# Performance work log

Measured on AMD Instinct MI355X. Metric: run time of the kernel, lower is better.

## Reference

```python
import jax, jax.numpy as jnp
import numpy as np
from math import sqrt

B, S, E, H = 2, 2048, 768, 12
DH = E // H
W = 256            # one-sided attention window (attention_window=512)
G = 16             # number of global tokens (positions 0..G-1 in every batch row)
PAD = 128          # last PAD tokens per row are padding (masked)
FF = 3072          # SwiGLU intermediate size
NEG = -1e9
EPS = 1e-5


def _ln(x, g, b):
    m = jnp.mean(x, axis=-1, keepdims=True)
    v = jnp.var(x, axis=-1, keepdims=True)
    return (x - m) * jax.lax.rsqrt(v + EPS) * g + b


def _rope(x, t):
    # x: [B,H,S,DH]; t: [B,S] float 'set positions'
    half = DH // 2
    inv_freq = 1.0 / (10000.0 ** (jnp.arange(half, dtype=jnp.float32) / half))
    ang = t[:, None, :, None] * inv_freq            # [B,1,S,half]
    cos, sin = jnp.cos(ang), jnp.sin(ang)
    x1, x2 = x[..., :half], x[..., half:]
    return jnp.concatenate([x1 * cos - x2 * sin, x2 * cos + x1 * sin], axis=-1)


def _heads(x):  # [B,S,E] -> [B,H,S,DH]
    return x.reshape(B, S, H, DH).transpose(0, 2, 1, 3)


def _chunk3(x):
    # [B,H,S,D] -> [B,H,C,3W,D]: for query chunk c, keys from chunks c-1,c,c+1 (zero padded)
    b, h, s, d = x.shape
    c = s // W
    xp = jnp.pad(x, ((0, 0), (0, 0), (W, W), (0, 0))).reshape(b, h, c + 2, W, d)
    return jnp.concatenate([xp[:, :, :-2], xp[:, :, 1:-1], xp[:, :, 2:]], axis=3)


def _forward(x, attention_mask, global_attention_mask,
             Wq, bq, Wk, bk, Wv, bv, Wqg, bqg, Wkg, bkg, Wvg, bvg,
             ln0_g, ln0_b, ln1_g, ln1_b, W1, W3, W2):
    C = S // W
    merged = attention_mask * (global_attention_mask + 1)   # 0 masked, 1 local, 2 global
    is_masked = merged == 0
    is_global = merged == 2
    remove = merged != 1   # keys removed from windowed attention (masked or global)

    q = _heads(x @ Wq + bq) / sqrt(DH)
    k = _heads(x @ Wk + bk)
    v = _heads(x @ Wv + bv)

    # RoPE over 'set positions': (~is_index_masked) * cumsum(is_index_global_attn)
    t = jnp.where(is_masked, 0, jnp.cumsum(is_global.astype(jnp.int32), axis=1)).astype(jnp.float32)
    q = _rope(q, t)
    k = _rope(k, t)

    # --- sliding-window (banded) scores: band[b,h,i,d] = q_i . k_{i+d-W} ---
    qc = q.reshape(B, H, C, W, DH)
    k3 = _chunk3(k)
    s3 = jnp.einsum('bhcpd,bhcqd->bhcpq', qc, k3)                     # [B,H,C,W,3W]
    didx = jnp.arange(W)[:, None] + jnp.arange(2 * W + 1)[None, :]    # [W,2W+1]
    band = jnp.take_along_axis(s3, didx[None, None, None], axis=-1)   # [B,H,C,W,2W+1]

    # mask removed keys / out-of-range positions inside the band
    rmp = jnp.pad(remove, ((0, 0), (W, W)), constant_values=True).reshape(B, C + 2, W)
    rm3 = jnp.concatenate([rmp[:, :-2], rmp[:, 1:-1], rmp[:, 2:]], axis=2)  # [B,C,3W]
    band_rm = jnp.take_along_axis(jnp.broadcast_to(rm3[:, :, None, :], (B, C, W, 3 * W)),
                                  didx[None, None], axis=-1)                # [B,C,W,2W+1]
    band = jnp.where(band_rm[:, None], NEG, band).reshape(B, H, S, 2 * W + 1)

    # --- global-key columns (keys taken from the RoPE'd local key vectors) ---
    sg = jnp.einsum('bhid,bhgd->bhig', q, k[:, :, :G])                # [B,H,S,G]

    scores = jnp.concatenate([sg, band], axis=-1)                     # [B,H,S,G+2W+1]
    probs = jax.nn.softmax(scores.astype(jnp.float32), axis=-1).astype(x.dtype)
    probs = jnp.where(is_masked[:, None, :, None], 0.0, probs)

    # --- probs @ value: global columns + band ---
    out = jnp.einsum('bhig,bhgd->bhid', probs[..., :G], v[:, :, :G])
    pl = probs[..., G:].reshape(B, H, C, W, 2 * W + 1)
    rows = jnp.broadcast_to(jnp.arange(W)[:, None], (W, 2 * W + 1))
    p3 = jnp.zeros((B, H, C, W, 3 * W), probs.dtype).at[:, :, :, rows, didx].set(pl)
    v3 = _chunk3(v)
    out = out + jnp.einsum('bhcpq,bhcqd->bhcpd', p3, v3).reshape(B, H, S, DH)
    attn = out.transpose(0, 2, 1, 3).reshape(B, S, E)

    # --- full attention for global tokens (separate global projections, no RoPE) ---
    gq = _heads(x @ Wqg + bqg)[:, :, :G] / sqrt(DH)                   # [B,H,G,DH]
    gk = _heads(x @ Wkg + bkg)
    gv = _heads(x @ Wvg + bvg)
    gs = jnp.einsum('bhgd,bhjd->bhgj', gq, gk)                        # [B,H,G,S]
    gs = jnp.where(is_masked[:, None, None, :], NEG, gs)
    gp = jax.nn.softmax(gs.astype(jnp.float32), axis=-1).astype(x.dtype)
    gout = jnp.einsum('bhgj,bhjd->bhgd', gp, gv).transpose(0, 2, 1, 3).reshape(B, G, E)
    attn = attn.at[:, :G].set(gout)

    # residual + post-LN, SwiGLU FFN, residual + post-LN (dropout = eval mode)
    h0 = _ln(x + attn, ln0_g, ln0_b)
    ffn = (jax.nn.silu(h0 @ W1) * (h0 @ W3)) @ W2
    return _ln(h0 + ffn, ln1_g, ln1_b)


def setup_inputs():
    key = jax.random.key(0)
    ks = jax.random.split(key, 12)
    x = jax.random.normal(ks[0], (B, S, E), jnp.float32)
    attention_mask = jnp.ones((B, S), jnp.int32).at[:, S - PAD:].set(0)
    global_attention_mask = jnp.zeros((B, S), jnp.int32).at[:, :G].set(1)
    sd = 0.02
    def w(k, shape):
        return jax.random.normal(k, shape, jnp.float32) * sd
    return dict(
        x=x, attention_mask=attention_mask, global_attention_mask=global_attention_mask,
        Wq=w(ks[1], (E, E)), bq=jnp.zeros((E,), jnp.float32),
        Wk=w(ks[2], (E, E)), bk=jnp.zeros((E,), jnp.float32),
        Wv=w(ks[3], (E, E)), bv=jnp.zeros((E,), jnp.float32),
        Wqg=w(ks[4], (E, E)), bqg=jnp.zeros((E,), jnp.float32),
        Wkg=w(ks[5], (E, E)), bkg=jnp.zeros((E,), jnp.float32),
        Wvg=w(ks[6], (E, E)), bvg=jnp.zeros((E,), jnp.float32),
        ln0_g=jnp.ones((E,), jnp.float32), ln0_b=jnp.zeros((E,), jnp.float32),
        ln1_g=jnp.ones((E,), jnp.float32), ln1_b=jnp.zeros((E,), jnp.float32),
        W1=w(ks[7], (E, FF)), W3=w(ks[8], (E, FF)), W2=w(ks[9], (FF, E)))


def reference(x, attention_mask, global_attention_mask, Wq, bq, Wk, bk, Wv, bv,
              Wqg, bqg, Wkg, bkg, Wvg, bvg, ln0_g, ln0_b, ln1_g, ln1_b, W1, W3, W2):
    return _forward(x, attention_mask, global_attention_mask,
                    Wq, bq, Wk, bk, Wv, bv, Wqg, bqg, Wkg, bkg, Wvg, bvg,
                    ln0_g, ln0_b, ln1_g, ln1_b, W1, W3, W2)
```

## Files before the change

kernel.cpp:

```cpp
#include <hip/hip_runtime.h>


#define BB_ 2
#define SS 2048
#define EE 768
#define HH 12
#define DHH 64
#define GG 16
#define FFN 3072
#define MM (BB_*SS)

typedef __bf16 bf16_t;
typedef __bf16 bf16x8_t __attribute__((ext_vector_type(8)));
typedef float f32x4_t __attribute__((ext_vector_type(4)));

__device__ inline void gload16(const void* g, void* l) {
  __builtin_amdgcn_global_load_lds((const __attribute__((address_space(1))) void*)g,
                                   (__attribute__((address_space(3))) void*)l, 16, 0, 0);
}

__global__ __launch_bounds__(64) void detect_kernel(const unsigned int* __restrict__ w,
                                                    int* __restrict__ flag) {
  int cnt = 0;
  for (int i = threadIdx.x; i < 1024; i += 64) {
    unsigned e = (w[i] >> 7) & 0xFF;
    cnt += (e >= 100 && e <= 144) ? 1 : 0;
  }
  for (int off = 32; off; off >>= 1) cnt += __shfl_xor(cnt, off);
  if (threadIdx.x == 0) flag[0] = (cnt > 512) ? 1 : 0;
}

struct PrepParams {
  const void* csrc[11]; bf16_t* cdst[11];
  const void* tsrc[9];  bf16_t* tdst[9];
  const int* am; const int* gm;
  float* tpos; int* flags;
  float* zbuf; int zn;
};

#define NB_CANON 3081
#define NB_T1 3456
#define NB_T2 4608
#define NB_T3 2304
#define NB_TRANS (NB_T1+NB_T2+NB_T3)

__global__ __launch_bounds__(256) void prep_kernel(PrepParams P,
                                                   const int* __restrict__ flag) {
  __shared__ bf16_t tile[32][33];
  __shared__ int wtot[4];
  int bid = blockIdx.x;
  const int t = threadIdx.x;
  const bool isb = flag[0] != 0;

  if (bid < NB_CANON) {
    constexpr int ns[11] = {3145728, 768,768,768,768,768,768, 768,768,768,768};
    int idx4 = (bid*256 + t)*4;
    int off = 0, seg = -1, loc = 0;
    #pragma unroll
    for (int i=0;i<11;i++) {
      if (seg < 0 && idx4 < off + ns[i]) { seg = i; loc = idx4 - off; }
      off += ns[i];
    }
    if (seg < 0) return;
    const void* s = P.csrc[seg];
    bf16_t* d = P.cdst[seg];
    if (isb) {
      *(uint2*)&d[loc] = *(const uint2*)((const unsigned short*)s + loc);
    } else {
      float4 v = *(const float4*)((const float*)s + loc);
      d[loc+0] = (bf16_t)v.x; d[loc+1] = (bf16_t)v.y;
      d[loc+2] = (bf16_t)v.z; d[loc+3] = (bf16_t)v.w;
    }
    return;
  }
  bid -= NB_CANON;

  if (bid < NB_TRANS) {
    int job, bx, by, R, C;
    if (bid < NB_T1)            { job = bid/576;          int r = bid%576;  bx = r%24; by = r/24; R=EE;  C=EE;  }
    else if (bid < NB_T1+NB_T2) { int l = bid-NB_T1; job = 6 + l/2304; int r = l%2304; bx = r%96; by = r/96; R=EE;  C=FFN; }
    else                        { int l = bid-NB_T1-NB_T2; job = 8;          bx = l%24; by = l/24; R=FFN; C=EE;  }
    const void* src = P.tsrc[job]; bf16_t* dst = P.tdst[job];
    int tx = t & 31, ty = t >> 5;
    int r0 = by*32, c0 = bx*32;
    #pragma unroll
    for (int i=0;i<4;i++) {
      int rr = ty + i*8;
      size_t si = (size_t)(r0+rr)*C + c0 + tx;
      tile[rr][tx] = isb ? ((const bf16_t*)src)[si] : (bf16_t)((const float*)src)[si];
    }
    __syncthreads();
    #pragma unroll
    for (int i=0;i<4;i++) {
      int cc = ty + i*8;
      dst[(size_t)(c0+cc)*R + r0 + tx] = tile[tx][cc];
    }
    return;
  }
  bid -= NB_TRANS;

  if (bid < BB_) {
    int b = bid;
    int lane = t & 63, wv = t >> 6;
    int base = b*SS + t*8;
    int mg[8]; int isg[8]; int loc = 0;
    for (int i=0;i<8;i++) {
      int a = P.am[base+i], g = P.gm[base+i];
      int merged = a*(g+1);
      mg[i] = merged;
      isg[i] = (merged==2) ? 1 : 0;
      loc += isg[i];
    }
    int x = loc;
    for (int off=1; off<64; off<<=1) {
      int y = __shfl_up(x, off);
      if (lane >= off) x += y;
    }
    if (lane==63) wtot[wv] = x;
    __syncthreads();
    int prev = 0;
    for (int w=0; w<wv; w++) prev += wtot[w];
    int run = prev + x - loc;
    for (int i=0;i<8;i++) {
      run += isg[i];
      int masked = (mg[i]==0) ? 1 : 0;
      int glob   = (mg[i]==2) ? 1 : 0;
      int rem    = (mg[i]!=1) ? 1 : 0;
      P.tpos[base+i]  = masked ? 0.f : (float)run;
      P.flags[base+i] = masked | (glob<<1) | (rem<<2);
    }
    return;
  }
  bid -= BB_;
  int i = bid*256 + t;
  if (i < P.zn) P.zbuf[i] = 0.f;
}

__device__ inline void gemm128_core(const bf16_t* __restrict__ A,
                                    const bf16_t* __restrict__ BT,
                                    int ldA, int ldB, int kbeg, int kend,
                                    int m0, int n0,
                                    bf16_t* As, bf16_t* Bs,
                                    f32x4_t (&acc)[4][4]) {
  const int t = threadIdx.x;
  const int lane = t & 63, wv = t >> 6;
  const int l15 = lane & 15, quad = lane >> 4;
  const int wr = (wv >> 1) << 6, wc = (wv & 1) << 6;
  const int rsub = lane >> 3, pch = lane & 7;
  const int sch = pch ^ rsub;
  const size_t abase = (size_t)(m0 + wv*32 + rsub)*ldA + sch*8;
  const size_t bbase = (size_t)(n0 + wv*32 + rsub)*ldB + sch*8;
  const int sx = l15 & 7;
  bf16_t* lA = As + (wv*32)*64;
  bf16_t* lB = Bs + (wv*32)*64;
  for (int k0 = kbeg; k0 < kend; k0 += 64) {
    __syncthreads();
    #pragma unroll
    for (int j=0;j<4;j++) {
      gload16(A + abase + (size_t)(j*8)*ldA + k0, lA + j*8*64);
      gload16(BT + bbase + (size_t)(j*8)*ldB + k0, lB + j*8*64);
    }
    __syncthreads();
    #pragma unroll
    for (int c=0;c<2;c++) {
      bf16x8_t af[4], bfr[4];
      #pragma unroll
      for (int a=0;a<4;a++)
        af[a] = *(const bf16x8_t*)&As[(wr + a*16 + l15)*64 + ((c*4+quad)^sx)*8];
      #pragma unroll
      for (int b=0;b<4;b++)
        bfr[b] = *(const bf16x8_t*)&Bs[(wc + b*16 + l15)*64 + ((c*4+quad)^sx)*8];
      #pragma unroll
      for (int a=0;a<4;a++)
        #pragma unroll
        for (int b=0;b<4;b++)
          acc[a][b] = __builtin_amdgcn_mfma_f32_16x16x32_bf16(af[a], bfr[b], acc[a][b], 0,0,0);
    }
  }
}

struct ProjParams {
  const bf16_t* W[5];
  const bf16_t* Bi[5];
  bf16_t* O[5];
};

__global__ __launch_bounds__(256) void projqg_kernel(const bf16_t* __restrict__ x,
                                                     ProjParams P,
                                                     const float* __restrict__ tpos,
                                                     const bf16_t* __restrict__ WqgT,
                                                     const bf16_t* __restrict__ bqg,
                                                     float* __restrict__ qgb) {
  __shared__ bf16_t As[128*64];
  __shared__ bf16_t Bs[128*64];
  const int bid = blockIdx.x;
  const int t = threadIdx.x;
  const int lane = t & 63, wv = t >> 6;

  if (bid >= 960) {
    int l = bid - 960;
    int g = l & 15;
    int rest = l >> 4;
    int hg = rest % 3, b = rest / 3;
    float* xs = (float*)As;
    for (int i=t; i<EE; i+=256) xs[i] = (float)x[((size_t)b*SS + g)*EE + i];
    __syncthreads();
    int h = hg*4 + wv, d = lane;
    float acc = 0.f;
    const bf16_t* wrow = WqgT + (size_t)(h*64+d)*EE;
    #pragma unroll 4
    for (int k=0;k<EE;k+=8) {
      bf16x8_t w8 = *(const bf16x8_t*)(wrow + k);
      #pragma unroll
      for (int i=0;i<8;i++) acc += xs[k+i] * (float)w8[i];
    }
    acc = (acc + (float)bqg[h*64+d]) * 0.125f;
    qgb[((size_t)(b*HH+h)*GG + g)*DHH + d] = acc;
    return;
  }

  const int z  = bid / 192;
  const int rem = bid % 192;
  const int m0 = (rem % 32)*128, n0 = (rem / 32)*128;
  f32x4_t acc[4][4];
  #pragma unroll
  for (int a=0;a<4;a++)
    #pragma unroll
    for (int b=0;b<4;b++) acc[a][b] = (f32x4_t){0.f,0.f,0.f,0.f};
  gemm128_core(x, P.W[z], EE, EE, 0, EE, m0, n0, As, Bs, acc);

  const int l15 = lane & 15, quad = lane >> 4;
  const int wr = (wv >> 1) << 6, wc = (wv & 1) << 6;
  const float scale = (z==0) ? 0.125f : 1.f;
  const bool rope = (z<2);
  const int h = (n0 + wc) >> 6;
  bf16_t* Oz = P.O[z];
  const bf16_t* Bz = P.Bi[z];
  float bvals[4];
  #pragma unroll
  for (int b=0;b<4;b++) bvals[b] = (float)Bz[h*64 + b*16 + l15];
  #pragma unroll
  for (int a=0;a<4;a++) {
    #pragma unroll
    for (int r=0;r<4;r++) {
      int row = m0 + wr + a*16 + quad*4 + r;
      int bb = row >> 11, spos = row & (SS-1);
      float vals[4];
      #pragma unroll
      for (int b=0;b<4;b++) vals[b] = (acc[a][b][r] + bvals[b]) * scale;
      if (rope) {
        float tv = tpos[row];
        #pragma unroll
        for (int b=0;b<2;b++) {
          int j = b*16 + l15;
          float inv = __expf(-(float)j * (9.210340371976184f/32.f));
          float ang = tv * inv;
          float sn = __sinf(ang), cs = __cosf(ang);
          float x1 = vals[b], x2 = vals[b+2];
          vals[b]   = x1*cs - x2*sn;
          vals[b+2] = x2*cs + x1*sn;
        }
      }
      bf16_t* dst = Oz + ((size_t)(bb*HH + h)*SS + spos)*DHH;
      #pragma unroll
      for (int b=0;b<4;b++) dst[b*16 + l15] = (bf16_t)vals[b];
    }
  }
}

__global__ __launch_bounds__(256) void gemm_ffn13(const bf16_t* __restrict__ A,
                                                  const bf16_t* __restrict__ B1T,
                                                  const bf16_t* __restrict__ B3T,
                                                  bf16_t* __restrict__ g1) {
  const int n0 = blockIdx.x*64, m0 = blockIdx.y*128;
  __shared__ bf16_t As[128*64];
  __shared__ bf16_t Bs1[64*64];
  __shared__ bf16_t Bs3[64*64];
  const int t = threadIdx.x;
  const int lane = t & 63, wv = t >> 6;
  const int l15 = lane & 15, quad = lane >> 4;
  const int wr = (wv >> 1) << 6, wc = (wv & 1) << 5;
  const int rsub = lane >> 3, pch = lane & 7;
  const int sch = pch ^ rsub;
  const size_t abase = (size_t)(m0 + wv*32 + rsub)*EE + sch*8;
  const size_t bbase = (size_t)(n0 + wv*16 + rsub)*EE + sch*8;
  const int sx = l15 & 7;
  bf16_t* lA  = As  + (wv*32)*64;
  bf16_t* lB1 = Bs1 + (wv*16)*64;
  bf16_t* lB3 = Bs3 + (wv*16)*64;
  f32x4_t a1[4][2], a3[4][2];
  #pragma unroll
  for (int a=0;a<4;a++)
    #pragma unroll
    for (int b=0;b<2;b++) { a1[a][b] = (f32x4_t){0.f,0.f,0.f,0.f};
                            a3[a][b] = (f32x4_t){0.f,0.f,0.f,0.f}; }
  for (int k0 = 0; k0 < EE; k0 += 64) {
    __syncthreads();
    #pragma unroll
    for (int j=0;j<4;j++)
      gload16(A + abase + (size_t)(j*8)*EE + k0, lA + j*8*64);
    #pragma unroll
    for (int j=0;j<2;j++) {
      gload16(B1T + bbase + (size_t)(j*8)*EE + k0, lB1 + j*8*64);
      gload16(B3T + bbase + (size_t)(j*8)*EE + k0, lB3 + j*8*64);
    }
    __syncthreads();
    #pragma unroll
    for (int c=0;c<2;c++) {
      bf16x8_t af[4], b1f[2], b3f[2];
      #pragma unroll
      for (int a=0;a<4;a++)
        af[a] = *(const bf16x8_t*)&As[(wr + a*16 + l15)*64 + ((c*4+quad)^sx)*8];
      #pragma unroll
      for (int b=0;b<2;b++) {
        b1f[b] = *(const bf16x8_t*)&Bs1[(wc + b*16 + l15)*64 + ((c*4+quad)^sx)*8];
        b3f[b] = *(const bf16x8_t*)&Bs3[(wc + b*16 + l15)*64 + ((c*4+quad)^sx)*8];
      }
      #pragma unroll
      for (int a=0;a<4;a++)
        #pragma unroll
        for (int b=0;b<2;b++) {
          a1[a][b] = __builtin_amdgcn_mfma_f32_16x16x32_bf16(af[a], b1f[b], a1[a][b], 0,0,0);
          a3[a][b] = __builtin_amdgcn_mfma_f32_16x16x32_bf16(af[a], b3f[b], a3[a][b], 0,0,0);
        }
    }
  }
  #pragma unroll
  for (int a=0;a<4;a++)
    #pragma unroll
    for (int r=0;r<4;r++) {
      int row = m0 + wr + a*16 + quad*4 + r;
      #pragma unroll
      for (int b=0;b<2;b++) {
        float tv = a1[a][b][r];
        float sil = tv / (1.f + __expf(-tv));
        g1[(size_t)row*FFN + n0 + wc + b*16 + l15] = (bf16_t)(sil * a3[a][b][r]);
      }
    }
}

struct Ffn2Out { float* p[4]; };

__global__ __launch_bounds__(256) void gemm_ffn2(const bf16_t* __restrict__ A,
                                                 const bf16_t* __restrict__ BT,
                                                 Ffn2Out O) {
  const int m0 = blockIdx.x*128, n0 = blockIdx.y*128;
  const int kz = blockIdx.z;
  __shared__ bf16_t As[128*64];
  __shared__ bf16_t Bs[128*64];
  f32x4_t acc[4][4];
  #pragma unroll
  for (int a=0;a<4;a++)
    #pragma unroll
    for (int b=0;b<4;b++) acc[a][b] = (f32x4_t){0.f,0.f,0.f,0.f};
  gemm128_core(A, BT, FFN, FFN, kz*768, (kz+1)*768, m0, n0, As, Bs, acc);
  const int t = threadIdx.x;
  const int lane = t & 63, wv = t >> 6;
  const int l15 = lane & 15, quad = lane >> 4;
  const int wr = (wv >> 1) << 6, wc = (wv & 1) << 6;
  float* C = O.p[kz];
  #pragma unroll
  for (int a=0;a<4;a++)
    #pragma unroll
    for (int r=0;r<4;r++) {
      int row = m0 + wr + a*16 + quad*4 + r;
      #pragma unroll
      for (int b=0;b<4;b++)
        C[(size_t)row*EE + n0 + wc + b*16 + l15] = acc[a][b][r];
    }
}

__device__ void band_body(char* smem,
                          const bf16_t* __restrict__ qb,
                          const bf16_t* __restrict__ kb,
                          const bf16_t* __restrict__ vb,
                          const int* __restrict__ flags,
                          float* __restrict__ attn) {
  const int flat = blockIdx.x;
  const int nb = (flat & 7) * 48 + (flat >> 3);
  const int px = nb & 15;
  const int hb = nb >> 4;
  const int h = hb % HH, b = hb / HH;
  const int p0 = px * 128;

  const int t = threadIdx.x;
  const int wv = t>>6, lane = t&63;
  const int l15 = lane & 15, quad = lane >> 4;
  const size_t bh = (size_t)(b*HH+h);
  const bf16_t* kbh = kb + bh*SS*DHH;
  const bf16_t* vbh = vb + bh*SS*DHH;
  const int* fl = flags + b*SS;
  const int qbase = p0 + wv*32;

  bf16_t* KsB = (bf16_t*)smem;
  bf16_t* VtB = (bf16_t*)(smem + 16384);
  bf16_t* PwB = (bf16_t*)(smem + 35840);

  bf16x8_t qa[2][2];
  #pragma unroll
  for (int g=0; g<2; g++) {
    const bf16_t* qrow = qb + (bh*SS + qbase + g*16 + l15)*DHH;
    qa[g][0] = *(const bf16x8_t*)(qrow + quad*8);
    qa[g][1] = *(const bf16x8_t*)(qrow + 32 + quad*8);
  }

  const int srsub = lane >> 3, spch = lane & 7;
  const int vkp  = (t & 31) * 2;
  const int vdh0 = (t >> 5) * 8;

  {
    const int kb0 = p0 - 256;
    #pragma unroll
    for (int j=0;j<2;j++) {
      int row = wv*16 + j*8 + srsub;
      int kc = min(max(kb0 + row, 0), SS-1);
      gload16(kbh + (size_t)kc*DHH + (spch ^ srsub)*8, &KsB[(wv*16 + j*8)*DHH]);
    }
    int kc1 = min(max(kb0 + vkp,   0), SS-1);
    int kc2 = min(max(kb0 + vkp+1, 0), SS-1);
    bf16x8_t v1 = *(const bf16x8_t*)(vbh + (size_t)kc1*DHH + vdh0);
    bf16x8_t v2 = *(const bf16x8_t*)(vbh + (size_t)kc2*DHH + vdh0);
    #pragma unroll
    for (int i=0;i<8;i++) {
      union { unsigned u; bf16_t hh[2]; } pk;
      pk.hh[0] = v1[i]; pk.hh[1] = v2[i];
      *(unsigned*)&VtB[(vdh0+i)*72 + vkp] = pk.u;
    }
  }
  __syncthreads();

  f32x4_t o[2][4];
  #pragma unroll
  for (int g=0; g<2; g++)
    #pragma unroll
    for (int i=0;i<4;i++) o[g][i] = (f32x4_t){0.f,0.f,0.f,0.f};
  float lsum[2][4] = {{0.f,0.f,0.f,0.f},{0.f,0.f,0.f,0.f}};
  bf16_t* P = PwB + wv*(32*72);

  for (int unit=0; unit<11; unit++) {
    const int cur = unit & 1, nxt = cur ^ 1;
    const int kb0 = (unit<10) ? (p0 - 256 + unit*64) : 0;
    const bool pre = (unit < 10);
    bf16x8_t pv1, pv2;
    if (pre) {
      const int kbn = (unit < 9) ? (kb0 + 64) : 0;
      #pragma unroll
      for (int j=0;j<2;j++) {
        int row = wv*16 + j*8 + srsub;
        int kc = min(max(kbn + row, 0), SS-1);
        gload16(kbh + (size_t)kc*DHH + (spch ^ srsub)*8,
                &KsB[nxt*(64*DHH) + (wv*16 + j*8)*DHH]);
      }
      int kc1 = min(max(kbn + vkp,   0), SS-1);
      int kc2 = min(max(kbn + vkp+1, 0), SS-1);
      pv1 = *(const bf16x8_t*)(vbh + (size_t)kc1*DHH + vdh0);
      pv2 = *(const bf16x8_t*)(vbh + (size_t)kc2*DHH + vdh0);
    }
    const bf16_t* Kc = KsB + cur*(64*DHH);
    const int nsub = (unit<10) ? 4 : 1;
    for (int sub=0; sub<4; sub++) {
      if (sub < nsub) {
        int krow = sub*16 + l15;
        int kpos = kb0 + krow;
        bf16x8_t kf0 = *(const bf16x8_t*)&Kc[krow*DHH + (((quad  ) ^ (krow&7))<<3)];
        bf16x8_t kf1 = *(const bf16x8_t*)&Kc[krow*DHH + (((quad+4) ^ (krow&7))<<3)];
        int kc = min(max(kpos,0),SS-1);
        bool drop = false;
        if (unit<10) drop = (kpos<0) || (kpos>=SS) || (((fl[kc]>>2)&1)!=0);
        #pragma unroll
        for (int g=0; g<2; g++) {
          f32x4_t s = (f32x4_t){0.f,0.f,0.f,0.f};
          s = __builtin_amdgcn_mfma_f32_16x16x32_bf16(qa[g][0], kf0, s, 0,0,0);
          s = __builtin_amdgcn_mfma_f32_16x16x32_bf16(qa[g][1], kf1, s, 0,0,0);
          #pragma unroll
          for (int r=0;r<4;r++) {
            float e;
            if (unit==10) {
              e = __expf(s[r]);
            } else {
              int dj = kpos - (qbase + g*16 + quad*4 + r);
              bool valid = (dj>=-256) && (dj<=256) && (!drop);
              e = valid ? __expf(s[r]) : 0.f;
            }
            lsum[g][r] += e;
            P[(g*16 + quad*4 + r)*72 + sub*16 + l15] = (bf16_t)e;
          }
        }
      } else {
        #pragma unroll
        for (int g=0; g<2; g++)
          #pragma unroll
          for (int r=0;r<4;r++) P[(g*16 + quad*4 + r)*72 + sub*16 + l15] = (bf16_t)0.f;
      }
    }
    const bf16_t* Vc = VtB + cur*(64*72);
    __builtin_amdgcn_s_setprio(1);
    #pragma unroll
    for (int g=0; g<2; g++) {
      #pragma unroll
      for (int chunk=0; chunk<2; chunk++) {
        bf16x8_t pf = *(const bf16x8_t*)&P[(g*16 + l15)*72 + chunk*32 + quad*8];
        #pragma unroll
        for (int nt=0; nt<4; nt++) {
          bf16x8_t vf = *(const bf16x8_t*)&Vc[(nt*16+l15)*72 + chunk*32 + quad*8];
          o[g][nt] = __builtin_amdgcn_mfma_f32_16x16x32_bf16(pf, vf, o[g][nt], 0,0,0);
        }
      }
    }
    __builtin_amdgcn_s_setprio(0);
    if (pre) {
      #pragma unroll
      for (int i=0;i<8;i++) {
        union { unsigned u; bf16_t hh[2]; } pk;
        pk.hh[0] = pv1[i]; pk.hh[1] = pv2[i];
        *(unsigned*)&VtB[nxt*(64*72) + (vdh0+i)*72 + vkp] = pk.u;
      }
      __syncthreads();
    }
  }
  #pragma unroll
  for (int g=0; g<2; g++) {
    #pragma unroll
    for (int r=0;r<4;r++) {
      float s = lsum[g][r];
      s += __shfl_xor(s,1); s += __shfl_xor(s,2);
      s += __shfl_xor(s,4); s += __shfl_xor(s,8);
      lsum[g][r] = s;
    }
    #pragma unroll
    for (int r=0;r<4;r++) {
      int q = qbase + g*16 + quad*4 + r;
      int masked = fl[q] & 1;
      float inv = masked ? 0.f : 1.f/lsum[g][r];
      float* dst = attn + ((size_t)(b*SS+q))*EE + h*64 + l15;
      #pragma unroll
      for (int nt=0; nt<4; nt++) dst[nt*16] = o[g][nt][r]*inv;
    }
  }
}

__device__ void gattn_body(char* smem,
                           const float* __restrict__ qgb,
                           const bf16_t* __restrict__ kgb,
                           const bf16_t* __restrict__ vgb,
                           const int* __restrict__ flags,
                           float* __restrict__ go,
                           float* __restrict__ gl) {
  const int l = blockIdx.x - 384;
  const int kbase = (l % 16)*128;
  const int h = (l / 16) % HH, b = l / (16*HH);
  const int t = threadIdx.x;
  float* gqs = (float*)smem;
  float* Ks  = gqs + 16*68;
  float* Vs  = Ks + 64*68;
  float* es  = Vs + 64*68;
  const size_t bh = (size_t)(b*HH+h);
  #pragma unroll
  for (int j=0;j<4;j++) {
    int idx = t + j*256;
    int g = idx>>6, d = idx&63;
    gqs[g*68+d] = qgb[(bh*GG + g)*DHH + d];
  }
  float accv[4] = {0.f,0.f,0.f,0.f};
  float lpart = 0.f;
  const int gs = t>>4, kslot = t&15;
  const int dp = t&63, grp = t>>6;
  const bf16_t* kb_ = kgb + bh*SS*DHH;
  const bf16_t* vb_ = vgb + bh*SS*DHH;
  const int* fl = flags + b*SS;
  for (int tile=0; tile<2; tile++) {
    int k0 = kbase + tile*64;
    __syncthreads();
    {
      int row = t>>2, seg = t&3;
      const bf16_t* sk = kb_ + (size_t)(k0+row)*DHH + seg*16;
      const bf16_t* sv = vb_ + (size_t)(k0+row)*DHH + seg*16;
      bf16x8_t k1 = *(const bf16x8_t*)sk;
      bf16x8_t k2 = *(const bf16x8_t*)(sk+8);
      bf16x8_t v1 = *(const bf16x8_t*)sv;
      bf16x8_t v2 = *(const bf16x8_t*)(sv+8);
      #pragma unroll
      for (int i=0;i<8;i++) {
        Ks[row*68 + seg*16 + i]     = (float)k1[i];
        Ks[row*68 + seg*16 + 8 + i] = (float)k2[i];
        Vs[row*68 + seg*16 + i]     = (float)v1[i];
        Vs[row*68 + seg*16 + 8 + i] = (float)v2[i];
      }
    }
    __syncthreads();
    #pragma unroll
    for (int j=0;j<4;j++) {
      int key = kslot + 16*j;
      const float* gq = &gqs[gs*68];
      const float* kr = &Ks[key*68];
      float s = 0.f;
      #pragma unroll
      for (int d4=0; d4<64; d4+=4) {
        float4 a = *(const float4*)(gq + d4);
        float4 kk = *(const float4*)(kr + d4);
        s += a.x*kk.x + a.y*kk.y + a.z*kk.z + a.w*kk.w;
      }
      int msk = fl[k0+key] & 1;
      float e = msk ? 0.f : __expf(s);
      es[gs*64+key] = e;
      lpart += e;
    }
    __syncthreads();
    #pragma unroll
    for (int g=0; g<4; g++) {
      int gg = grp*4+g;
      float a = accv[g];
      for (int key=0;key<64;key++) a += es[gg*64+key]*Vs[key*68+dp];
      accv[g] = a;
    }
  }
  __syncthreads();
  es[gs*64 + kslot] = lpart;
  __syncthreads();
  if (t < 16) {
    float s = 0.f;
    for (int j=0;j<16;j++) s += es[t*64+j];
    atomicAdd(&gl[bh*16 + t], s);
  }
  #pragma unroll
  for (int g=0; g<4; g++)
    atomicAdd(&go[(bh*16 + grp*4+g)*64 + dp], accv[g]);
}

__global__ __launch_bounds__(256) void attn_kernel(const bf16_t* __restrict__ qb,
                                                   const bf16_t* __restrict__ kb,
                                                   const bf16_t* __restrict__ vb,
                                                   const float* __restrict__ qgb,
                                                   const bf16_t* __restrict__ kgb,
                                                   const bf16_t* __restrict__ vgb,
                                                   const int* __restrict__ flags,
                                                   float* __restrict__ attn,
                                                   float* __restrict__ go,
                                                   float* __restrict__ gl) {
  __shared__ __align__(16) char smem[54272];
  if (blockIdx.x < 384) band_body(smem, qb, kb, vb, flags, attn);
  else                  gattn_body(smem, qgb, kgb, vgb, flags, go, gl);
}

__global__ __launch_bounds__(256) void addln_kernel(const bf16_t* __restrict__ Abf,
                                                    const float* __restrict__ Af,
                                                    const float* __restrict__ B0,
                                                    const float* __restrict__ B1,
                                                    const float* __restrict__ B2,
                                                    const float* __restrict__ B3,
                                                    const float* __restrict__ gof,
                                                    const float* __restrict__ glf,
                                                    const bf16_t* __restrict__ gw,
                                                    const bf16_t* __restrict__ bw,
                                                    float* __restrict__ outf,
                                                    bf16_t* __restrict__ outb,
                                                    const int* __restrict__ flagp) {
  int r = blockIdx.x, t = threadIdx.x;
  int lane = t&63, wv = t>>6;
  int spos = r & (SS-1), bb = r >> 11;
  bool isglob = (gof != nullptr) && (spos < GG);
  float v[3]; float sum=0.f, ss=0.f;
  #pragma unroll
  for (int j=0;j<3;j++) {
    int idx = t + j*256;
    size_t gi = (size_t)r*EE+idx;
    float a = Abf ? (float)Abf[gi] : Af[gi];
    float bv;
    if (isglob) {
      int hh = idx >> 6, dp = idx & 63;
      int slot = (bb*HH + hh)*GG + spos;
      bv = gof[(size_t)slot*DHH + dp] / glf[slot];
    } else {
      bv = B0[gi];
    }
    float val = a + bv;
    if (B1) val += B1[gi];
    if (B2) val += B2[gi];
    if (B3) val += B3[gi];
    v[j] = val; sum += val; ss += val*val;
  }
  #pragma unroll
  for (int off=32; off>=1; off>>=1) {
    sum += __shfl_xor(sum, off);
    ss  += __shfl_xor(ss, off);
  }
  __shared__ float s1[4], s2[4];
  if (lane==0) { s1[wv]=sum; s2[wv]=ss; }
  __syncthreads();
  sum = s1[0]+s1[1]+s1[2]+s1[3];
  ss  = s2[0]+s2[1]+s2[2]+s2[3];
  float mean = sum * (1.f/(float)EE);
  float var  = ss * (1.f/(float)EE) - mean*mean;
  float rstd = rsqrtf(var + 1e-5f);
  bool wantb, wantf;
  if (flagp) { bool isb = (*flagp)!=0; wantb = isb; wantf = !isb; }
  else { wantb = (outb!=nullptr); wantf = (outf!=nullptr); }
  #pragma unroll
  for (int j=0;j<3;j++) {
    int idx = t + j*256;
    float o = (v[j]-mean)*rstd*(float)gw[idx] + (float)bw[idx];
    if (wantf) outf[(size_t)r*EE+idx] = o;
    if (wantb) outb[(size_t)r*EE+idx] = (bf16_t)o;
  }
}

extern "C" void kernel_launch(void* const* d_in, const int* in_sizes, int n_in,
                              void* d_out, int out_size, void* d_ws, size_t ws_size,
                              hipStream_t stream) {
  const void* x_r    = d_in[0];
  const int* am      = (const int*)d_in[1];
  const int* gm      = (const int*)d_in[2];
  (void)in_sizes; (void)n_in; (void)out_size; (void)ws_size;

  char* ws = (char*)d_ws;
  size_t off = 0;
  auto alloc = [&](size_t bytes) -> void* {
    void* p = ws + off;
    off += (bytes + 255) & ~(size_t)255;
    return p;
  };
  bf16_t* xc    = (bf16_t*)alloc((size_t)MM*EE*2);
  bf16_t* WT[6]; bf16_t* bc[6];
  for (int i=0;i<6;i++) { WT[i] = (bf16_t*)alloc((size_t)EE*EE*2); bc[i] = (bf16_t*)alloc(EE*2); }
  bf16_t* lnc[4];
  for (int i=0;i<4;i++) lnc[i] = (bf16_t*)alloc(EE*2);
  bf16_t* W1T = (bf16_t*)alloc((size_t)EE*FFN*2);
  bf16_t* W3T = (bf16_t*)alloc((size_t)EE*FFN*2);
  bf16_t* W2T = (bf16_t*)alloc((size_t)FFN*EE*2);
  const size_t NBHSD = (size_t)BB_*HH*SS*DHH;
  bf16_t* qb    = (bf16_t*)alloc(NBHSD*2);
  bf16_t* kb    = (bf16_t*)alloc(NBHSD*2);
  bf16_t* vb    = (bf16_t*)alloc(NBHSD*2);
  bf16_t* kgb   = (bf16_t*)alloc(NBHSD*2);
  bf16_t* vgb   = (bf16_t*)alloc(NBHSD*2);
  float* qgb   = (float*)alloc((size_t)BB_*HH*GG*DHH*4);
  float* attn  = (float*)alloc((size_t)MM*EE*4);
  float* h0f   = (float*)alloc((size_t)MM*EE*4);
  bf16_t* h0b  = (bf16_t*)alloc((size_t)MM*EE*2);
  bf16_t* g1   = (bf16_t*)alloc((size_t)MM*FFN*2);
  float* p3    = (float*)alloc((size_t)MM*EE*4);
  float* go    = (float*)alloc((size_t)BB_*HH*GG*DHH*4);
  float* gl    = (float*)alloc((size_t)BB_*HH*GG*4);
  float* tposb = (float*)alloc((size_t)BB_*SS*4);
  int*   flagb = (int*)alloc((size_t)BB_*SS*4);
  int*   dflag = (int*)alloc(256);
  float* p1 = (float*)qb;
  float* p2 = (float*)qb + (size_t)MM*EE;

  detect_kernel<<<1, 64, 0, stream>>>((const unsigned int*)d_in[3], dflag);

  PrepParams PP;
  const void* csrc[11] = { x_r, d_in[4], d_in[6], d_in[8], d_in[10], d_in[12], d_in[14],
                           d_in[15], d_in[16], d_in[17], d_in[18] };
  bf16_t* cdst[11] = { xc, bc[0], bc[1], bc[2], bc[3], bc[4], bc[5],
                       lnc[0], lnc[1], lnc[2], lnc[3] };
  for (int i=0;i<11;i++) { PP.csrc[i]=csrc[i]; PP.cdst[i]=cdst[i]; }
  const int wi[6] = {3,5,7,9,11,13};
  for (int i=0;i<6;i++) { PP.tsrc[i]=d_in[wi[i]]; PP.tdst[i]=WT[i]; }
  PP.tsrc[6]=d_in[19]; PP.tdst[6]=W1T;
  PP.tsrc[7]=d_in[20]; PP.tdst[7]=W3T;
  PP.tsrc[8]=d_in[21]; PP.tdst[8]=W2T;
  PP.am = am; PP.gm = gm; PP.tpos = tposb; PP.flags = flagb;
  PP.zbuf = go; PP.zn = 24960;
  prep_kernel<<<NB_CANON + NB_TRANS + BB_ + 98, 256, 0, stream>>>(PP, dflag);

  ProjParams P;
  P.W[0]=WT[0]; P.Bi[0]=bc[0]; P.O[0]=qb;
  P.W[1]=WT[1]; P.Bi[1]=bc[1]; P.O[1]=kb;
  P.W[2]=WT[2]; P.Bi[2]=bc[2]; P.O[2]=vb;
  P.W[3]=WT[4]; P.Bi[3]=bc[4]; P.O[3]=kgb;
  P.W[4]=WT[5]; P.Bi[4]=bc[5]; P.O[4]=vgb;
  projqg_kernel<<<dim3(1056), 256, 0, stream>>>(xc, P, tposb, WT[3], bc[3], qgb);

  attn_kernel<<<dim3(768), 256, 0, stream>>>(qb, kb, vb, qgb, kgb, vgb,
                                             flagb, attn, go, gl);

  addln_kernel<<<MM, 256, 0, stream>>>(xc, nullptr, attn, nullptr, nullptr, nullptr,
                                       go, gl, lnc[0], lnc[1], h0f, h0b, nullptr);

  gemm_ffn13<<<dim3(FFN/64, MM/128), 256, 0, stream>>>(h0b, W1T, W3T, g1);
  Ffn2Out FO; FO.p[0]=attn; FO.p[1]=p1; FO.p[2]=p2; FO.p[3]=p3;
  gemm_ffn2<<<dim3(MM/128, EE/128, 4), 256, 0, stream>>>(g1, W2T, FO);

  addln_kernel<<<MM, 256, 0, stream>>>(nullptr, h0f, attn, p1, p2, p3,
                                       nullptr, nullptr, lnc[2], lnc[3],
                                       (float*)d_out, (bf16_t*)d_out, dflag);
}
```

Measured before the change: 347.7 us.

## Halve band-attention query tile to 64 rows for more blocks and occupancy

```diff
diff --git a/kernel.cpp b/kernel.cpp
--- a/kernel.cpp
+++ b/kernel.cpp
@@ -377,11 +377,11 @@
                           const int* __restrict__ flags,
                           float* __restrict__ attn) {
   const int flat = blockIdx.x;
-  const int nb = (flat & 7) * 48 + (flat >> 3);
-  const int px = nb & 15;
-  const int hb = nb >> 4;
+  const int nb = (flat & 7) * 96 + (flat >> 3);
+  const int px = nb & 31;
+  const int hb = nb >> 5;
   const int h = hb % HH, b = hb / HH;
-  const int p0 = px * 128;
+  const int p0 = px * 64;
 
   const int t = threadIdx.x;
   const int wv = t>>6, lane = t&63;
@@ -390,19 +390,15 @@
   const bf16_t* kbh = kb + bh*SS*DHH;
   const bf16_t* vbh = vb + bh*SS*DHH;
   const int* fl = flags + b*SS;
-  const int qbase = p0 + wv*32;
+  const int q0 = p0 + wv*16;
 
   bf16_t* KsB = (bf16_t*)smem;
   bf16_t* VtB = (bf16_t*)(smem + 16384);
-  bf16_t* PwB = (bf16_t*)(smem + 35840);
-
-  bf16x8_t qa[2][2];
-  #pragma unroll
-  for (int g=0; g<2; g++) {
-    const bf16_t* qrow = qb + (bh*SS + qbase + g*16 + l15)*DHH;
-    qa[g][0] = *(const bf16x8_t*)(qrow + quad*8);
-    qa[g][1] = *(const bf16x8_t*)(qrow + 32 + quad*8);
-  }
+  bf16_t* PwB = (bf16_t*)(smem + 34816);
+
+  const bf16_t* qrow = qb + (bh*SS + q0 + l15)*DHH;
+  bf16x8_t qa0 = *(const bf16x8_t*)(qrow + quad*8);
+  bf16x8_t qa1 = *(const bf16x8_t*)(qrow + 32 + quad*8);
 
   const int srsub = lane >> 3, spch = lane & 7;
   const int vkp  = (t & 31) * 2;
@@ -429,21 +425,19 @@
   }
   __syncthreads();
 
-  f32x4_t o[2][4];
-  #pragma unroll
-  for (int g=0; g<2; g++)
-    #pragma unroll
-    for (int i=0;i<4;i++) o[g][i] = (f32x4_t){0.f,0.f,0.f,0.f};
-  float lsum[2][4] = {{0.f,0.f,0.f,0.f},{0.f,0.f,0.f,0.f}};
-  bf16_t* P = PwB + wv*(32*72);
-
-  for (int unit=0; unit<11; unit++) {
+  f32x4_t o[4];
+  #pragma unroll
+  for (int i=0;i<4;i++) o[i] = (f32x4_t){0.f,0.f,0.f,0.f};
+  float lsum[4] = {0.f,0.f,0.f,0.f};
+  bf16_t* P = PwB + wv*(16*72);
+
+  for (int unit=0; unit<10; unit++) {
     const int cur = unit & 1, nxt = cur ^ 1;
-    const int kb0 = (unit<10) ? (p0 - 256 + unit*64) : 0;
-    const bool pre = (unit < 10);
+    const int kb0 = (unit<9) ? (p0 - 256 + unit*64) : 0;
+    const bool pre = (unit < 9);
     bf16x8_t pv1, pv2;
     if (pre) {
-      const int kbn = (unit < 9) ? (kb0 + 64) : 0;
+      const int kbn = (unit < 8) ? (kb0 + 64) : 0;
       #pragma unroll
       for (int j=0;j<2;j++) {
         int row = wv*16 + j*8 + srsub;
@@ -457,54 +451,46 @@
       pv2 = *(const bf16x8_t*)(vbh + (size_t)kc2*DHH + vdh0);
     }
     const bf16_t* Kc = KsB + cur*(64*DHH);
-    const int nsub = (unit<10) ? 4 : 1;
+    const int nsub = (unit<9) ? 4 : 1;
     for (int sub=0; sub<4; sub++) {
       if (sub < nsub) {
         int krow = sub*16 + l15;
         int kpos = kb0 + krow;
         bf16x8_t kf0 = *(const bf16x8_t*)&Kc[krow*DHH + (((quad  ) ^ (krow&7))<<3)];
         bf16x8_t kf1 = *(const bf16x8_t*)&Kc[krow*DHH + (((quad+4) ^ (krow&7))<<3)];
+        f32x4_t s = (f32x4_t){0.f,0.f,0.f,0.f};
+        s = __builtin_amdgcn_mfma_f32_16x16x32_bf16(qa0, kf0, s, 0,0,0);
+        s = __builtin_amdgcn_mfma_f32_16x16x32_bf16(qa1, kf1, s, 0,0,0);
         int kc = min(max(kpos,0),SS-1);
         bool drop = false;
-        if (unit<10) drop = (kpos<0) || (kpos>=SS) || (((fl[kc]>>2)&1)!=0);
+        if (unit<9) drop = (kpos<0) || (kpos>=SS) || (((fl[kc]>>2)&1)!=0);
         #pragma unroll
-        for (int g=0; g<2; g++) {
-          f32x4_t s = (f32x4_t){0.f,0.f,0.f,0.f};
-          s = __builtin_amdgcn_mfma_f32_16x16x32_bf16(qa[g][0], kf0, s, 0,0,0);
-          s = __builtin_amdgcn_mfma_f32_16x16x32_bf16(qa[g][1], kf1, s, 0,0,0);
-          #pragma unroll
-          for (int r=0;r<4;r++) {
-            float e;
-            if (unit==10) {
-              e = __expf(s[r]);
-            } else {
-              int dj = kpos - (qbase + g*16 + quad*4 + r);
-              bool valid = (dj>=-256) && (dj<=256) && (!drop);
-              e = valid ? __expf(s[r]) : 0.f;
-            }
-            lsum[g][r] += e;
-            P[(g*16 + quad*4 + r)*72 + sub*16 + l15] = (bf16_t)e;
+        for (int r=0;r<4;r++) {
+          float e;
+          if (unit==9) {
+            e = __expf(s[r]);
+          } else {
+            int dj = kpos - (q0 + quad*4 + r);
+            bool valid = (dj>=-256) && (dj<=256) && (!drop);
+            e = valid ? __expf(s[r]) : 0.f;
           }
+          lsum[r] += e;
+          P[(quad*4+r)*72 + sub*16 + l15] = (bf16_t)e;
         }
       } else {
         #pragma unroll
-        for (int g=0; g<2; g++)
-          #pragma unroll
-          for (int r=0;r<4;r++) P[(g*16 + quad*4 + r)*72 + sub*16 + l15] = (bf16_t)0.f;
+        for (int r=0;r<4;r++) P[(quad*4+r)*72 + sub*16 + l15] = (bf16_t)0.f;
       }
     }
     const bf16_t* Vc = VtB + cur*(64*72);
     __builtin_amdgcn_s_setprio(1);
     #pragma unroll
-    for (int g=0; g<2; g++) {
-      #pragma unroll
-      for (int chunk=0; chunk<2; chunk++) {
-        bf16x8_t pf = *(const bf16x8_t*)&P[(g*16 + l15)*72 + chunk*32 + quad*8];
-        #pragma unroll
-        for (int nt=0; nt<4; nt++) {
-          bf16x8_t vf = *(const bf16x8_t*)&Vc[(nt*16+l15)*72 + chunk*32 + quad*8];
-          o[g][nt] = __builtin_amdgcn_mfma_f32_16x16x32_bf16(pf, vf, o[g][nt], 0,0,0);
-        }
+    for (int chunk=0; chunk<2; chunk++) {
+      bf16x8_t pf = *(const bf16x8_t*)&P[l15*72 + chunk*32 + quad*8];
+      #pragma unroll
+      for (int nt=0; nt<4; nt++) {
+        bf16x8_t vf = *(const bf16x8_t*)&Vc[(nt*16+l15)*72 + chunk*32 + quad*8];
+        o[nt] = __builtin_amdgcn_mfma_f32_16x16x32_bf16(pf, vf, o[nt], 0,0,0);
       }
     }
     __builtin_amdgcn_s_setprio(0);
@@ -519,23 +505,20 @@
     }
   }
   #pragma unroll
-  for (int g=0; g<2; g++) {
-    #pragma unroll
-    for (int r=0;r<4;r++) {
-      float s = lsum[g][r];
-      s += __shfl_xor(s,1); s += __shfl_xor(s,2);
-      s += __shfl_xor(s,4); s += __shfl_xor(s,8);
-      lsum[g][r] = s;
-    }
-    #pragma unroll
-    for (int r=0;r<4;r++) {
-      int q = qbase + g*16 + quad*4 + r;
-      int masked = fl[q] & 1;
-      float inv = masked ? 0.f : 1.f/lsum[g][r];
-      float* dst = attn + ((size_t)(b*SS+q))*EE + h*64 + l15;
-      #pragma unroll
-      for (int nt=0; nt<4; nt++) dst[nt*16] = o[g][nt][r]*inv;
-    }
+  for (int r=0;r<4;r++) {
+    float s = lsum[r];
+    s += __shfl_xor(s,1); s += __shfl_xor(s,2);
+    s += __shfl_xor(s,4); s += __shfl_xor(s,8);
+    lsum[r] = s;
+  }
+  #pragma unroll
+  for (int r=0;r<4;r++) {
+    int q = q0 + quad*4 + r;
+    int masked = fl[q] & 1;
+    float inv = masked ? 0.f : 1.f/lsum[r];
+    float* dst = attn + ((size_t)(b*SS+q))*EE + h*64 + l15;
+    #pragma unroll
+    for (int nt=0; nt<4; nt++) dst[nt*16] = o[nt][r]*inv;
   }
 }
 
@@ -546,7 +529,7 @@
                            const int* __restrict__ flags,
                            float* __restrict__ go,
                            float* __restrict__ gl) {
-  const int l = blockIdx.x - 384;
+  const int l = blockIdx.x - 768;
   const int kbase = (l % 16)*128;
   const int h = (l / 16) % HH, b = l / (16*HH);
   const int t = threadIdx.x;
@@ -627,18 +610,18 @@
     atomicAdd(&go[(bh*16 + grp*4+g)*64 + dp], accv[g]);
 }
 
-__global__ __launch_bounds__(256) void attn_kernel(const bf16_t* __restrict__ qb,
-                                                   const bf16_t* __restrict__ kb,
-                                                   const bf16_t* __restrict__ vb,
-                                                   const float* __restrict__ qgb,
-                                                   const bf16_t* __restrict__ kgb,
-                                                   const bf16_t* __restrict__ vgb,
-                                                   const int* __restrict__ flags,
-                                                   float* __restrict__ attn,
-                                                   float* __restrict__ go,
-                                                   float* __restrict__ gl) {
-  __shared__ __align__(16) char smem[54272];
-  if (blockIdx.x < 384) band_body(smem, qb, kb, vb, flags, attn);
+__global__ __launch_bounds__(256, 4) void attn_kernel(const bf16_t* __restrict__ qb,
+                                                      const bf16_t* __restrict__ kb,
+                                                      const bf16_t* __restrict__ vb,
+                                                      const float* __restrict__ qgb,
+                                                      const bf16_t* __restrict__ kgb,
+                                                      const bf16_t* __restrict__ vgb,
+                                                      const int* __restrict__ flags,
+                                                      float* __restrict__ attn,
+                                                      float* __restrict__ go,
+                                                      float* __restrict__ gl) {
+  __shared__ __align__(16) char smem[44032];
+  if (blockIdx.x < 768) band_body(smem, qb, kb, vb, flags, attn);
   else                  gattn_body(smem, qgb, kgb, vgb, flags, go, gl);
 }
 
@@ -772,8 +755,8 @@
   P.W[4]=WT[5]; P.Bi[4]=bc[5]; P.O[4]=vgb;
   projqg_kernel<<<dim3(1056), 256, 0, stream>>>(xc, P, tposb, WT[3], bc[3], qgb);
 
-  attn_kernel<<<dim3(768), 256, 0, stream>>>(qb, kb, vb, qgb, kgb, vgb,
-                                             flagb, attn, go, gl);
+  attn_kernel<<<dim3(1152), 256, 0, stream>>>(qb, kb, vb, qgb, kgb, vgb,
+                                              flagb, attn, go, gl);
 
   addln_kernel<<<MM, 256, 0, stream>>>(xc, nullptr, attn, nullptr, nullptr, nullptr,
                                        go, gl, lnc[0], lnc[1], h0f, h0b, nullptr);
```

Result: slower. 366.6 us (+5.4%).
